# Performance work log

Measured on AMD Instinct MI355X. Metric: run time of the kernel, lower is better.

## Reference

```python
import jax, jax.numpy as jnp
import numpy as np

ROUTINGS = 3


def squash(v):
    # squash along last axis: v/|v| * |v|^2/(1+|v|^2)
    norm = jnp.linalg.norm(v, axis=-1, keepdims=True)
    ns = norm * norm
    return v / norm * (ns / (1.0 + ns))


def setup_inputs() -> dict:
    key = jax.random.key(0)
    k1, k2 = jax.random.split(key)
    B, N, I, D, Din = 256, 10, 1152, 16, 8
    inputs = jax.random.normal(k1, (B, I, Din), dtype=jnp.float32)
    # glorot-uniform-ish init for W [N, I, D, Din]
    limit = np.sqrt(6.0 / (D + Din)).astype(np.float32)
    W = jax.random.uniform(k2, (N, I, D, Din), dtype=jnp.float32,
                           minval=-limit, maxval=limit)
    return {"inputs": inputs, "W": W}


def reference(inputs, W):
    # inputs: [B, I, Din], W: [N, I, D, Din]
    # u_hat[b,n,i,d] = sum_k W[n,i,d,k] * inputs[b,i,k]  (replaces tf.map_fn)
    u_hat = jnp.einsum('nidk,bik->bnid', W, inputs)  # [B, N, I, D]
    b = jnp.zeros(u_hat.shape[:3], dtype=u_hat.dtype)  # [B, N, I]
    outputs = None
    for r in range(ROUTINGS):
        c = jax.nn.softmax(b, axis=1)  # softmax over output capsules N
        outputs = squash(jnp.einsum('bni,bnid->bnd', c, u_hat))  # [B, N, D]
        if r < ROUTINGS - 1:
            # agreement: a[b,n,i] = <outputs[b,n,:], u_hat[b,n,i,:]>
            b = b + jnp.einsum('bnd,bnid->bni', outputs, u_hat)
    return outputs
```

## Files before the change

kernel.cpp:

```cpp
#include <hip/hip_runtime.h>
#include <hip/hip_bf16.h>
#include <stdint.h>


#define BN 256
#define NN 10
#define II 1152
#define DD 16
#define KK 8
#define NT 18
#define NCH 3
#define CHI 384

typedef unsigned short ushort_t;
typedef unsigned int uint_t;

__device__ __forceinline__ float bflo(uint_t u) {
    union { uint_t i; float f; } v; v.i = u << 16; return v.f;
}
__device__ __forceinline__ float bfhi(uint_t u) {
    union { uint_t i; float f; } v; v.i = u & 0xffff0000u; return v.f;
}
__device__ __forceinline__ uint_t pkbf(float lo, float hi) {
    __hip_bfloat162 h = __float22bfloat162_rn(make_float2(lo, hi));
    uint_t u; __builtin_memcpy(&u, &h, sizeof(u)); return u;
}

__global__ __launch_bounds__(256) void caps_uhat_s0(const float* __restrict__ xg,
                                                    const float* __restrict__ wg,
                                                    ushort_t* __restrict__ u,
                                                    float* __restrict__ part0,
                                                    int b0, int c4)
{
    __shared__ float redn[4][64][NN];
    const int tid = threadIdx.x;
    const int lane = tid & 63, wv = tid >> 6;
    const int dq = lane & 3, il = lane >> 2;
    const int nb8 = gridDim.x >> 3;
    const int L   = (blockIdx.x & 7) * nb8 + (blockIdx.x >> 3);
    const int it  = L / c4;
    const int bl  = (L - it * c4) * 4;
    const int i = it * 64 + wv * 16 + il;

    const bool h0 = (il & 1), h1 = (il >> 1) & 1, h2 = (il >> 2) & 1, h3 = (il >> 3) & 1;
    float* myred = &redn[wv][lane][0];

    float xv[4][8];
#pragma unroll
    for (int bb = 0; bb < 4; ++bb) {
        const float4* xp = (const float4*)(xg + ((size_t)(b0 + bl + bb) * II + i) * KK);
        float4 x0 = xp[0], x1 = xp[1];
        xv[bb][0] = x0.x; xv[bb][1] = x0.y; xv[bb][2] = x0.z; xv[bb][3] = x0.w;
        xv[bb][4] = x1.x; xv[bb][5] = x1.y; xv[bb][6] = x1.z; xv[bb][7] = x1.w;
    }

    for (int n = 0; n < NN; ++n) {
        const float4* wp = (const float4*)(wg + (size_t)(n * II + i) * (DD * KK)) + dq * 8;
        float4 w[8];
#pragma unroll
        for (int j = 0; j < 8; ++j) w[j] = wp[j];

        float s[4][4];
#pragma unroll
        for (int dj = 0; dj < 4; ++dj) {
            float4 wa = w[2 * dj], wb = w[2 * dj + 1];
#pragma unroll
            for (int bb = 0; bb < 4; ++bb) {
                s[bb][dj] = wa.x * xv[bb][0] + wa.y * xv[bb][1]
                          + wa.z * xv[bb][2] + wa.w * xv[bb][3]
                          + wb.x * xv[bb][4] + wb.y * xv[bb][5]
                          + wb.z * xv[bb][6] + wb.w * xv[bb][7];
            }
        }
#pragma unroll
        for (int bb = 0; bb < 4; ++bb) {
            uint2 q;
            q.x = pkbf(s[bb][0], s[bb][1]);
            q.y = pkbf(s[bb][2], s[bb][3]);
            *(uint2*)(u + (((size_t)(bl + bb) * NN + n) * II + i) * DD + dq * 4) = q;
        }
        float v8[8];
#pragma unroll
        for (int k = 0; k < 8; ++k) {
            float a0 = s[(2 * k) >> 2][(2 * k) & 3];
            float a1 = s[(2 * k + 1) >> 2][(2 * k + 1) & 3];
            float give = h0 ? a0 : a1;
            float got  = __shfl_xor(give, 4, 64);
            v8[k] = (h0 ? a1 : a0) + got;
        }
        float v4[4];
#pragma unroll
        for (int k = 0; k < 4; ++k) {
            float a0 = v8[2 * k], a1 = v8[2 * k + 1];
            float give = h1 ? a0 : a1;
            float got  = __shfl_xor(give, 8, 64);
            v4[k] = (h1 ? a1 : a0) + got;
        }
        float v2[2];
#pragma unroll
        for (int k = 0; k < 2; ++k) {
            float a0 = v4[2 * k], a1 = v4[2 * k + 1];
            float give = h2 ? a0 : a1;
            float got  = __shfl_xor(give, 16, 64);
            v2[k] = (h2 ? a1 : a0) + got;
        }
        {
            float a0 = v2[0], a1 = v2[1];
            float give = h3 ? a0 : a1;
            float got  = __shfl_xor(give, 32, 64);
            myred[n] = (h3 ? a1 : a0) + got;
        }
    }
    __syncthreads();
#pragma unroll
    for (int idx = tid; idx < 640; idx += 256) {
        int bb = idx / 160, r = idx - bb * 160;
        int n = r >> 4, d = r & 15;
        int lane2 = ((bb * 4 + (d & 3)) << 2) + (d >> 2);
        float v = redn[0][lane2][n] + redn[1][lane2][n]
                + redn[2][lane2][n] + redn[3][lane2][n];
        part0[((size_t)(b0 + bl + bb) * NT + it) * 160 + r] = 0.1f * v;
    }
}

__device__ __forceinline__ void block_reduce_part(float sp[NN][4], int tid,
                                                  float* red,
                                                  float* __restrict__ partp)
{
#pragma unroll
    for (int m = 4; m <= 32; m <<= 1)
#pragma unroll
        for (int n = 0; n < NN; ++n)
#pragma unroll
            for (int j = 0; j < 4; ++j)
                sp[n][j] += __shfl_xor(sp[n][j], m, 64);

    const int lane = tid & 63, wv = tid >> 6, ld = tid & 3;
    if (lane < 4) {
#pragma unroll
        for (int n = 0; n < NN; ++n)
#pragma unroll
            for (int j = 0; j < 4; ++j)
                red[(wv * NN + n) * 16 + ld * 4 + j] = sp[n][j];
    }
    __syncthreads();
    if (tid < 160) {
        int n = tid >> 4, dd = tid & 15;
        float v = 0.f;
#pragma unroll
        for (int w = 0; w < 4; ++w) v += red[(w * NN + n) * 16 + dd];
        partp[tid] = v;
    }
}

__global__ __launch_bounds__(256) void caps_sweep(const ushort_t* __restrict__ u,
                                                  const float* __restrict__ p0,
                                                  const float* __restrict__ p1,
                                                  float* __restrict__ pout, int b0)
{
    __shared__ float red[4 * 160];
    __shared__ float o_s[160];
    const int tid = threadIdx.x, g = tid >> 2, ld = tid & 3;
    const int cb = blockIdx.x / NCH, ch = blockIdx.x % NCH;
    const int b = b0 + cb;
    const ushort_t* ub = u + (size_t)cb * (NN * II * DD);

    if (tid < 160) {
        float v = 0.f;
#pragma unroll
        for (int t = 0; t < NT; ++t)
            v += p0[((size_t)b * NT + t) * 160 + tid];
        float sq = v * v;
#pragma unroll
        for (int m = 1; m <= 8; m <<= 1) sq += __shfl_xor(sq, m, 64);
        float o = v * (sqrtf(sq) / (1.0f + sq));
        if (p1) {
            float v1 = 0.f;
#pragma unroll
            for (int c2 = 0; c2 < NCH; ++c2)
                v1 += p1[((size_t)b * NCH + c2) * 160 + tid];
            float sq1 = v1 * v1;
#pragma unroll
            for (int m = 1; m <= 8; m <<= 1) sq1 += __shfl_xor(sq1, m, 64);
            o += v1 * (sqrtf(sq1) / (1.0f + sq1));
        }
        o_s[tid] = o;
    }
    __syncthreads();

    float sp[NN][4];
#pragma unroll
    for (int n = 0; n < NN; ++n)
#pragma unroll
        for (int j = 0; j < 4; ++j) sp[n][j] = 0.f;

    for (int step = 0; step < CHI / 64; ++step) {
        int i = ch * CHI + step * 64 + g;
        uint2 r[NN];
#pragma unroll
        for (int n = 0; n < NN; ++n)
            r[n] = *(const uint2*)(ub + ((size_t)(n * II + i)) * DD + ld * 4);

        float p[NN];
#pragma unroll
        for (int n = 0; n < NN; ++n) {
            float4 o4 = *(const float4*)&o_s[(n << 4) + (ld << 2)];
            p[n] = bflo(r[n].x) * o4.x + bfhi(r[n].x) * o4.y
                 + bflo(r[n].y) * o4.z + bfhi(r[n].y) * o4.w;
        }
        float a[NN];
#pragma unroll
        for (int n = 0; n < NN; ++n) {
            float t2 = p[n] + __shfl_xor(p[n], 1, 64);
            a[n] = t2 + __shfl_xor(t2, 2, 64);
        }
        float m = a[0];
#pragma unroll
        for (int n = 1; n < NN; ++n) m = fmaxf(m, a[n]);
        float c[NN], ssum = 0.f;
#pragma unroll
        for (int n = 0; n < NN; ++n) { c[n] = __expf(a[n] - m); ssum += c[n]; }
        float inv = 1.0f / ssum;
#pragma unroll
        for (int n = 0; n < NN; ++n) {
            float w = c[n] * inv;
            sp[n][0] += w * bflo(r[n].x); sp[n][1] += w * bfhi(r[n].x);
            sp[n][2] += w * bflo(r[n].y); sp[n][3] += w * bfhi(r[n].y);
        }
    }
    block_reduce_part(sp, tid, red, pout + ((size_t)b * NCH + ch) * 160);
}

__global__ __launch_bounds__(192) void caps_out(const float* __restrict__ p2,
                                                float* __restrict__ out, int b0)
{
    const int b = b0 + blockIdx.x;
    const int t = threadIdx.x;
    if (t < 160) {
        float v = 0.f;
#pragma unroll
        for (int ch = 0; ch < NCH; ++ch)
            v += p2[((size_t)b * NCH + ch) * 160 + t];
        float sq = v * v;
#pragma unroll
        for (int m = 1; m <= 8; m <<= 1) sq += __shfl_xor(sq, m, 64);
        out[(size_t)b * 160 + t] = v * (sqrtf(sq) / (1.0f + sq));
    }
}

extern "C" void kernel_launch(void* const* d_in, const int* in_sizes, int n_in,
                              void* d_out, int out_size, void* d_ws, size_t ws_size,
                              hipStream_t stream)
{
    const float* xg = (const float*)d_in[0];
    const float* wg = (const float*)d_in[1];
    if (n_in >= 2 && in_sizes[0] == NN * II * DD * KK) {
        const float* t = xg; xg = wg; wg = t;
    }
    float* outp = (float*)d_out;

    const size_t perB  = (size_t)NN * II * DD * 2;
    const size_t p0B   = (size_t)BN * NT * 160 * 4;
    const size_t p12B  = (size_t)BN * NCH * 160 * 4;
    size_t extra = p0B + 2 * p12B;
    size_t avail = (ws_size > extra) ? ws_size - extra : 0;
    int C = 256;
    if (avail < (size_t)256 * perB) {
        C = (int)(avail / perB);
        C &= ~15;
        if (C < 16) C = 16;
    }
    ushort_t* uws = (ushort_t*)d_ws;
    float* part0 = (float*)((char*)d_ws + (size_t)C * perB);
    float* part1 = part0 + (size_t)BN * NT * 160;
    float* part2 = part1 + (size_t)BN * NCH * 160;

    for (int b0 = 0; b0 < BN; b0 += C) {
        int c = (BN - b0 < C) ? (BN - b0) : C;
        int c4 = c / 4;
        caps_uhat_s0<<<NT * c4, 256, 0, stream>>>(xg, wg, uws, part0, b0, c4);
        caps_sweep  <<<c * NCH, 256, 0, stream>>>(uws, part0, nullptr, part1, b0);
        caps_sweep  <<<c * NCH, 256, 0, stream>>>(uws, part0, part1,  part2, b0);
        caps_out    <<<c,       192, 0, stream>>>(part2, outp, b0);
    }
}
```

Baseline: 154.7 us.

## Split u_hat kernel over capsule pairs, finer sweep chunks, hoist squash into kernel

The u_hat kernel's grid now covers pairs of output capsules, so each block handles 2 of the 10 capsules and there are five times as many blocks. The sweep kernels use 9 chunks of 128 inputs instead of 3 of 384, with the step loop unrolled. The per-batch squash of partial sums moves out of every sweep block into a small separate kernel, so each batch's output vector is computed once instead of once per chunk. The goal is more parallelism and less redundant prologue work, at the cost of two extra launches, repeated x loads across capsule pairs, and more partial sums to reduce.

After: 170.3 us. 10.1% more time.

```diff
diff --git a/kernel.cpp b/kernel.cpp
--- a/kernel.cpp
+++ b/kernel.cpp
@@ -9,8 +9,9 @@
 #define DD 16
 #define KK 8
 #define NT 18
-#define NCH 3
-#define CHI 384
+#define NP 5
+#define NCH 9
+#define CHI 128
 
 typedef unsigned short ushort_t;
 typedef unsigned int uint_t;
@@ -32,14 +33,17 @@
                                                     float* __restrict__ part0,
                                                     int b0, int c4)
 {
-    __shared__ float redn[4][64][NN];
+    __shared__ float redn[4][64][2];
     const int tid = threadIdx.x;
     const int lane = tid & 63, wv = tid >> 6;
     const int dq = lane & 3, il = lane >> 2;
     const int nb8 = gridDim.x >> 3;
     const int L   = (blockIdx.x & 7) * nb8 + (blockIdx.x >> 3);
-    const int it  = L / c4;
-    const int bl  = (L - it * c4) * 4;
+    const int it  = L / (NP * c4);
+    const int rem = L - it * (NP * c4);
+    const int np  = rem / c4;
+    const int bl  = (rem - np * c4) * 4;
+    const int n0  = np * 2;
     const int i = it * 64 + wv * 16 + il;
 
     const bool h0 = (il & 1), h1 = (il >> 1) & 1, h2 = (il >> 2) & 1, h3 = (il >> 3) & 1;
@@ -54,7 +58,9 @@
         xv[bb][4] = x1.x; xv[bb][5] = x1.y; xv[bb][6] = x1.z; xv[bb][7] = x1.w;
     }
 
-    for (int n = 0; n < NN; ++n) {
+#pragma unroll
+    for (int nn = 0; nn < 2; ++nn) {
+        const int n = n0 + nn;
         const float4* wp = (const float4*)(wg + (size_t)(n * II + i) * (DD * KK)) + dq * 8;
         float4 w[8];
 #pragma unroll
@@ -108,18 +114,45 @@
             float a0 = v2[0], a1 = v2[1];
             float give = h3 ? a0 : a1;
             float got  = __shfl_xor(give, 32, 64);
-            myred[n] = (h3 ? a1 : a0) + got;
+            myred[nn] = (h3 ? a1 : a0) + got;
         }
     }
     __syncthreads();
-#pragma unroll
-    for (int idx = tid; idx < 640; idx += 256) {
-        int bb = idx / 160, r = idx - bb * 160;
-        int n = r >> 4, d = r & 15;
+    if (tid < 128) {
+        int bb = tid >> 5, r5 = tid & 31, nn = r5 >> 4, d = r5 & 15;
         int lane2 = ((bb * 4 + (d & 3)) << 2) + (d >> 2);
-        float v = redn[0][lane2][n] + redn[1][lane2][n]
-                + redn[2][lane2][n] + redn[3][lane2][n];
-        part0[((size_t)(b0 + bl + bb) * NT + it) * 160 + r] = 0.1f * v;
+        float v = redn[0][lane2][nn] + redn[1][lane2][nn]
+                + redn[2][lane2][nn] + redn[3][lane2][nn];
+        part0[((size_t)(b0 + bl + bb) * NT + it) * 160 + (n0 + nn) * 16 + d] = 0.1f * v;
+    }
+}
+
+__global__ __launch_bounds__(192) void caps_o(const float* __restrict__ p0,
+                                              const float* __restrict__ p1,
+                                              float* __restrict__ og, int b0)
+{
+    const int b = b0 + blockIdx.x;
+    const int t = threadIdx.x;
+    if (t < 160) {
+        float v = 0.f;
+#pragma unroll
+        for (int tt = 0; tt < NT; ++tt)
+            v += p0[((size_t)b * NT + tt) * 160 + t];
+        float sq = v * v;
+#pragma unroll
+        for (int m = 1; m <= 8; m <<= 1) sq += __shfl_xor(sq, m, 64);
+        float o = v * (sqrtf(sq) / (1.0f + sq));
+        if (p1) {
+            float v1 = 0.f;
+#pragma unroll
+            for (int c2 = 0; c2 < NCH; ++c2)
+                v1 += p1[((size_t)b * NCH + c2) * 160 + t];
+            float sq1 = v1 * v1;
+#pragma unroll
+            for (int m = 1; m <= 8; m <<= 1) sq1 += __shfl_xor(sq1, m, 64);
+            o += v1 * (sqrtf(sq1) / (1.0f + sq1));
+        }
+        og[(size_t)b * 160 + t] = o;
     }
 }
 
@@ -154,8 +187,7 @@
 }
 
 __global__ __launch_bounds__(256) void caps_sweep(const ushort_t* __restrict__ u,
-                                                  const float* __restrict__ p0,
-                                                  const float* __restrict__ p1,
+                                                  const float* __restrict__ og,
                                                   float* __restrict__ pout, int b0)
 {
     __shared__ float red[4 * 160];
@@ -165,27 +197,7 @@
     const int b = b0 + cb;
     const ushort_t* ub = u + (size_t)cb * (NN * II * DD);
 
-    if (tid < 160) {
-        float v = 0.f;
-#pragma unroll
-        for (int t = 0; t < NT; ++t)
-            v += p0[((size_t)b * NT + t) * 160 + tid];
-        float sq = v * v;
-#pragma unroll
-        for (int m = 1; m <= 8; m <<= 1) sq += __shfl_xor(sq, m, 64);
-        float o = v * (sqrtf(sq) / (1.0f + sq));
-        if (p1) {
-            float v1 = 0.f;
-#pragma unroll
-            for (int c2 = 0; c2 < NCH; ++c2)
-                v1 += p1[((size_t)b * NCH + c2) * 160 + tid];
-            float sq1 = v1 * v1;
-#pragma unroll
-            for (int m = 1; m <= 8; m <<= 1) sq1 += __shfl_xor(sq1, m, 64);
-            o += v1 * (sqrtf(sq1) / (1.0f + sq1));
-        }
-        o_s[tid] = o;
-    }
+    if (tid < 160) o_s[tid] = og[(size_t)b * 160 + tid];
     __syncthreads();
 
     float sp[NN][4];
@@ -194,6 +206,7 @@
 #pragma unroll
         for (int j = 0; j < 4; ++j) sp[n][j] = 0.f;
 
+#pragma unroll
     for (int step = 0; step < CHI / 64; ++step) {
         int i = ch * CHI + step * 64 + g;
         uint2 r[NN];
@@ -262,7 +275,8 @@
     const size_t perB  = (size_t)NN * II * DD * 2;
     const size_t p0B   = (size_t)BN * NT * 160 * 4;
     const size_t p12B  = (size_t)BN * NCH * 160 * 4;
-    size_t extra = p0B + 2 * p12B;
+    const size_t oB    = (size_t)BN * 160 * 4;
+    size_t extra = p0B + 2 * p12B + 2 * oB;
     size_t avail = (ws_size > extra) ? ws_size - extra : 0;
     int C = 256;
     if (avail < (size_t)256 * perB) {
@@ -274,13 +288,17 @@
     float* part0 = (float*)((char*)d_ws + (size_t)C * perB);
     float* part1 = part0 + (size_t)BN * NT * 160;
     float* part2 = part1 + (size_t)BN * NCH * 160;
+    float* o1    = part2 + (size_t)BN * NCH * 160;
+    float* o2    = o1 + (size_t)BN * 160;
 
     for (int b0 = 0; b0 < BN; b0 += C) {
         int c = (BN - b0 < C) ? (BN - b0) : C;
         int c4 = c / 4;
-        caps_uhat_s0<<<NT * c4, 256, 0, stream>>>(xg, wg, uws, part0, b0, c4);
-        caps_sweep  <<<c * NCH, 256, 0, stream>>>(uws, part0, nullptr, part1, b0);
-        caps_sweep  <<<c * NCH, 256, 0, stream>>>(uws, part0, part1,  part2, b0);
-        caps_out    <<<c,       192, 0, stream>>>(part2, outp, b0);
-    }
-}
+        caps_uhat_s0<<<NT * NP * c4, 256, 0, stream>>>(xg, wg, uws, part0, b0, c4);
+        caps_o      <<<c, 192, 0, stream>>>(part0, nullptr, o1, b0);
+        caps_sweep  <<<c * NCH, 256, 0, stream>>>(uws, o1, part1, b0);
+        caps_o      <<<c, 192, 0, stream>>>(part0, part1, o2, b0);
+        caps_sweep  <<<c * NCH, 256, 0, stream>>>(uws, o2, part2, b0);
+        caps_out    <<<c, 192, 0, stream>>>(part2, outp, b0);
+    }
+}
```

## Split u_hat kernel over capsule pairs with LDS-staged W and prefetch sweep loads

Applied to the files above, without the earlier changes.

The u_hat kernel now runs five times as many blocks, each handling two output capsules instead of all ten. W tiles are staged asynchronously into swizzled LDS with global_load_lds, and the second capsule's load is double-buffered behind compute of the first. The sweep kernel software-pipelines its bf16 u_hat loads by fetching the next step's rows while computing the current one. These changes add parallelism and hide memory latency, at the cost of more registers and reloading x per block.

New measurement: 141.3 us. -8.7%, faster.

```diff
diff --git a/kernel.cpp b/kernel.cpp
--- a/kernel.cpp
+++ b/kernel.cpp
@@ -9,6 +9,7 @@
 #define DD 16
 #define KK 8
 #define NT 18
+#define NP 5
 #define NCH 3
 #define CHI 384
 
@@ -32,18 +33,41 @@
                                                     float* __restrict__ part0,
                                                     int b0, int c4)
 {
-    __shared__ float redn[4][64][NN];
+    __shared__ float wlds[4][2048];
+    __shared__ float redn[4][64][2];
     const int tid = threadIdx.x;
     const int lane = tid & 63, wv = tid >> 6;
     const int dq = lane & 3, il = lane >> 2;
     const int nb8 = gridDim.x >> 3;
     const int L   = (blockIdx.x & 7) * nb8 + (blockIdx.x >> 3);
-    const int it  = L / c4;
-    const int bl  = (L - it * c4) * 4;
+    const int it  = L / (NP * c4);
+    const int rem = L - it * (NP * c4);
+    const int np  = rem / c4;
+    const int bl  = (rem - np * c4) * 4;
+    const int n0  = np * 2;
     const int i = it * 64 + wv * 16 + il;
 
     const bool h0 = (il & 1), h1 = (il >> 1) & 1, h2 = (il >> 2) & 1, h3 = (il >> 3) & 1;
     float* myred = &redn[wv][lane][0];
+    float* mylds = &wlds[wv][0];
+    const int lrow = lane >> 5, lc = lane & 31;
+    const float4* wtile0 = (const float4*)(wg + (size_t)(n0 * II + it * 64 + wv * 16) * (DD * KK));
+
+#define STAGE_W(NNV)                                                         \
+    {                                                                        \
+        const float4* wt = wtile0 + (size_t)(NNV) * II * 32;                 \
+        _Pragma("unroll")                                                    \
+        for (int j = 0; j < 8; ++j) {                                        \
+            int row = lrow + 2 * j;                                          \
+            int chunk = row * 32 + (lc ^ (row & 7));                         \
+            __builtin_amdgcn_global_load_lds(                                \
+                (const __attribute__((address_space(1))) void*)(wt + chunk), \
+                (__attribute__((address_space(3))) void*)(mylds + j * 256),  \
+                16, 0, 0);                                                   \
+        }                                                                    \
+    }
+
+    STAGE_W(0);
 
     float xv[4][8];
 #pragma unroll
@@ -54,12 +78,7 @@
         xv[bb][4] = x1.x; xv[bb][5] = x1.y; xv[bb][6] = x1.z; xv[bb][7] = x1.w;
     }
 
-    for (int n = 0; n < NN; ++n) {
-        const float4* wp = (const float4*)(wg + (size_t)(n * II + i) * (DD * KK)) + dq * 8;
-        float4 w[8];
-#pragma unroll
-        for (int j = 0; j < 8; ++j) w[j] = wp[j];
-
+    auto compute_n = [&](int n, const float4* w, int slot) {
         float s[4][4];
 #pragma unroll
         for (int dj = 0; dj < 4; ++dj) {
@@ -108,18 +127,33 @@
             float a0 = v2[0], a1 = v2[1];
             float give = h3 ? a0 : a1;
             float got  = __shfl_xor(give, 32, 64);
-            myred[n] = (h3 ? a1 : a0) + got;
-        }
-    }
+            myred[slot] = (h3 ? a1 : a0) + got;
+        }
+    };
+
+    float4 w[8];
+    asm volatile("s_waitcnt vmcnt(0)" ::: "memory");
+#pragma unroll
+    for (int jj = 0; jj < 8; ++jj)
+        w[jj] = *(const float4*)(mylds + il * 128 + dq * 32 + ((jj ^ (il & 7)) << 2));
+    asm volatile("s_waitcnt lgkmcnt(0)" ::: "memory");
+    STAGE_W(1);
+    compute_n(n0, w, 0);
+
+    asm volatile("s_waitcnt vmcnt(0)" ::: "memory");
+#pragma unroll
+    for (int jj = 0; jj < 8; ++jj)
+        w[jj] = *(const float4*)(mylds + il * 128 + dq * 32 + ((jj ^ (il & 7)) << 2));
+    compute_n(n0 + 1, w, 1);
+#undef STAGE_W
+
     __syncthreads();
-#pragma unroll
-    for (int idx = tid; idx < 640; idx += 256) {
-        int bb = idx / 160, r = idx - bb * 160;
-        int n = r >> 4, d = r & 15;
+    if (tid < 128) {
+        int bb = tid >> 5, r5 = tid & 31, nn = r5 >> 4, d = r5 & 15;
         int lane2 = ((bb * 4 + (d & 3)) << 2) + (d >> 2);
-        float v = redn[0][lane2][n] + redn[1][lane2][n]
-                + redn[2][lane2][n] + redn[3][lane2][n];
-        part0[((size_t)(b0 + bl + bb) * NT + it) * 160 + r] = 0.1f * v;
+        float v = redn[0][lane2][nn] + redn[1][lane2][nn]
+                + redn[2][lane2][nn] + redn[3][lane2][nn];
+        part0[((size_t)(b0 + bl + bb) * NT + it) * 160 + (n0 + nn) * 16 + d] = 0.1f * v;
     }
 }
 
@@ -165,6 +199,12 @@
     const int b = b0 + cb;
     const ushort_t* ub = u + (size_t)cb * (NN * II * DD);
 
+    const int i0 = ch * CHI + g;
+    uint2 r[NN];
+#pragma unroll
+    for (int n = 0; n < NN; ++n)
+        r[n] = *(const uint2*)(ub + ((size_t)(n * II + i0)) * DD + ld * 4);
+
     if (tid < 160) {
         float v = 0.f;
 #pragma unroll
@@ -194,12 +234,15 @@
 #pragma unroll
         for (int j = 0; j < 4; ++j) sp[n][j] = 0.f;
 
+#pragma unroll
     for (int step = 0; step < CHI / 64; ++step) {
-        int i = ch * CHI + step * 64 + g;
-        uint2 r[NN];
-#pragma unroll
-        for (int n = 0; n < NN; ++n)
-            r[n] = *(const uint2*)(ub + ((size_t)(n * II + i)) * DD + ld * 4);
+        uint2 rn[NN];
+        if (step + 1 < CHI / 64) {
+            const int i2 = i0 + (step + 1) * 64;
+#pragma unroll
+            for (int n = 0; n < NN; ++n)
+                rn[n] = *(const uint2*)(ub + ((size_t)(n * II + i2)) * DD + ld * 4);
+        }
 
         float p[NN];
 #pragma unroll
@@ -226,6 +269,10 @@
             float w = c[n] * inv;
             sp[n][0] += w * bflo(r[n].x); sp[n][1] += w * bfhi(r[n].x);
             sp[n][2] += w * bflo(r[n].y); sp[n][3] += w * bfhi(r[n].y);
+        }
+        if (step + 1 < CHI / 64) {
+#pragma unroll
+            for (int n = 0; n < NN; ++n) r[n] = rn[n];
         }
     }
     block_reduce_part(sp, tid, red, pout + ((size_t)b * NCH + ch) * 160);
@@ -278,7 +325,7 @@
     for (int b0 = 0; b0 < BN; b0 += C) {
         int c = (BN - b0 < C) ? (BN - b0) : C;
         int c4 = c / 4;
-        caps_uhat_s0<<<NT * c4, 256, 0, stream>>>(xg, wg, uws, part0, b0, c4);
+        caps_uhat_s0<<<NT * NP * c4, 256, 0, stream>>>(xg, wg, uws, part0, b0, c4);
         caps_sweep  <<<c * NCH, 256, 0, stream>>>(uws, part0, nullptr, part1, b0);
         caps_sweep  <<<c * NCH, 256, 0, stream>>>(uws, part0, part1,  part2, b0);
         caps_out    <<<c,       192, 0, stream>>>(part2, outp, b0);
```
